# Kernel optimization log

Measured on AMD Instinct MI355X. Metric: run time of the kernel, lower is better.

The kernel has to match this reference:

```python
import jax, jax.numpy as jnp
import numpy as np

KH = KW = 3
STRIDE = 1
PAD = 1
DIL = 1
G = 4  # deformable groups


def setup_inputs() -> dict:
    key = jax.random.key(0)
    k1, k2, k3 = jax.random.split(key, 3)
    B, C, H, W = 8, 256, 64, 64
    K = KH * KW
    inp = jax.random.normal(k1, (B, C, H, W), dtype=jnp.float32)
    offset = jax.random.normal(k2, (B, 2 * G * K, H, W), dtype=jnp.float32)
    mask = jax.random.uniform(k3, (B, G * K, H, W), dtype=jnp.float32)
    return {"input": inp, "offset": offset, "mask": mask}


def _deform_sample(x, offset, mask):
    # x: [B,C,H,W]; offset: [B,2*G*K,Ho,Wo]; mask: [B,G*K,Ho,Wo]
    B, C, H, W = x.shape
    K = KH * KW
    Ho = (H + 2 * PAD - DIL * (KH - 1) - 1) // STRIDE + 1
    Wo = (W + 2 * PAD - DIL * (KW - 1) - 1) // STRIDE + 1
    Cg = C // G

    off = offset.reshape(B, G, K, 2, Ho, Wo)  # (dy, dx) per group/tap
    m = mask.reshape(B, G, K, Ho, Wo)

    # base sampling grid per kernel tap
    ky = (jnp.arange(KH) * DIL).repeat(KW)          # [K]
    kx = jnp.tile(jnp.arange(KW) * DIL, KH)          # [K]
    base_y = jnp.arange(Ho) * STRIDE - PAD           # [Ho]
    base_x = jnp.arange(Wo) * STRIDE - PAD           # [Wo]

    # sampling positions [B,G,K,Ho,Wo]
    py = base_y[None, None, None, :, None] + ky[None, None, :, None, None] + off[:, :, :, 0]
    px = base_x[None, None, None, None, :] + kx[None, None, :, None, None] + off[:, :, :, 1]

    y0 = jnp.floor(py).astype(jnp.int32)
    x0 = jnp.floor(px).astype(jnp.int32)
    ly = py - y0.astype(py.dtype)
    lx = px - x0.astype(px.dtype)

    xg = x.reshape(B, G, Cg, H * W)

    def gather(yy, xx, w):
        valid = (yy >= 0) & (yy < H) & (xx >= 0) & (xx < W)
        idx = jnp.clip(yy, 0, H - 1) * W + jnp.clip(xx, 0, W - 1)  # [B,G,K,Ho,Wo]
        g = jnp.take_along_axis(xg, idx.reshape(B, G, 1, -1), axis=3)
        g = g.reshape(B, G, Cg, K, Ho, Wo)
        return g * (w * valid.astype(w.dtype))[:, :, None]

    acc = gather(y0, x0, (1 - ly) * (1 - lx))
    acc = acc + gather(y0, x0 + 1, (1 - ly) * lx)
    acc = acc + gather(y0 + 1, x0, ly * (1 - lx))
    acc = acc + gather(y0 + 1, x0 + 1, ly * lx)

    # mask-weighted accumulation over kernel taps
    out = (acc * m[:, :, None]).sum(axis=3)  # [B,G,Cg,Ho,Wo]
    return out.reshape(B, C, Ho, Wo)


def reference(input, offset, mask):
    return _deform_sample(input, offset, mask)
```

## Files before the change

kernel.cpp:

```cpp
#include <hip/hip_runtime.h>
#include <hip/hip_fp16.h>

#define B_  8
#define C_  256
#define H_  64
#define W_  64
#define G_  4
#define CG_ 64
#define K_  9
#define HW_ (H_ * W_)

__global__ __launch_bounds__(256) void to_ghwc_f16(const float* __restrict__ in,
                                                   __half* __restrict__ out) {
  __shared__ unsigned int tile[32][65];
  const int b  = blockIdx.z;
  const int p0 = blockIdx.x * 64;
  const int g  = blockIdx.y;
  const int tid = threadIdx.x;
  const float* src = in + (size_t)b * C_ * HW_ + (size_t)g * CG_ * HW_;
  __half* dst = out + ((size_t)(b * G_ + g) * HW_) * CG_;

  const int px  = tid & 63;
  const int cp0 = tid >> 6;
#pragma unroll
  for (int i = 0; i < 8; ++i) {
    const int cp = cp0 + i * 4;
    const int c  = cp * 2;
    const float v0 = src[(size_t)c * HW_ + p0 + px];
    const float v1 = src[(size_t)(c + 1) * HW_ + p0 + px];
    const unsigned int lo = (unsigned int)__half_as_ushort(__float2half(v0));
    const unsigned int hi = (unsigned int)__half_as_ushort(__float2half(v1));
    tile[cp][px] = lo | (hi << 16);
  }
  __syncthreads();

  const int cpair = tid & 31;
  const int pr0   = tid >> 5;
#pragma unroll
  for (int i = 0; i < 8; ++i) {
    const int p = pr0 + i * 8;
    *(unsigned int*)(dst + (size_t)(p0 + p) * CG_ + 2 * cpair) = tile[cpair][p];
  }
}

union DeformSM {
  struct { int4 o[576]; float4 w[576]; } p;
  float ot[64][65];
};

__global__ __launch_bounds__(256) void deform_g16(const __half* __restrict__ x,
                                                  const float* __restrict__ off,
                                                  const float* __restrict__ msk,
                                                  float* __restrict__ out) {
  __shared__ DeformSM sm;

  const int ho  = blockIdx.x;
  const int b   = blockIdx.y >> 2;
  const int g   = blockIdx.y & 3;
  const int tid = threadIdx.x;

  for (int e = tid; e < 576; e += 256) {
    const int px = e & 63;
    const int k  = e >> 6;
    const int ky = k / 3, kx = k - ky * 3;
    const int och = (g * K_ + k) * 2;
    const size_t ob = ((size_t)(b * (2 * G_ * K_) + och) * HW_) + ho * W_ + px;
    const float dy = off[ob];
    const float dx = off[ob + HW_];
    const float m  = msk[((size_t)(b * (G_ * K_) + g * K_ + k) * HW_) + ho * W_ + px];

    const float py = (float)(ho - 1 + ky) + dy;
    const float pxx = (float)(px - 1 + kx) + dx;
    const float fy = floorf(py), fx = floorf(pxx);
    const int y0 = (int)fy, x0 = (int)fx;
    const int y1 = y0 + 1,  x1 = x0 + 1;
    const float ly = py - fy, lx = pxx - fx;

    const bool vy0 = ((unsigned)y0 < (unsigned)H_), vy1 = ((unsigned)y1 < (unsigned)H_);
    const bool vx0 = ((unsigned)x0 < (unsigned)W_), vx1 = ((unsigned)x1 < (unsigned)W_);
    const float wy0 = (1.f - ly) * m, wy1 = ly * m;

    float4 w;
    w.x = (vy0 && vx0) ? wy0 * (1.f - lx) : 0.f;
    w.y = (vy0 && vx1) ? wy0 * lx         : 0.f;
    w.z = (vy1 && vx0) ? wy1 * (1.f - lx) : 0.f;
    w.w = (vy1 && vx1) ? wy1 * lx         : 0.f;

    const int y0c = min(max(y0, 0), H_ - 1), y1c = min(max(y1, 0), H_ - 1);
    const int x0c = min(max(x0, 0), W_ - 1), x1c = min(max(x1, 0), W_ - 1);

    int4 o;
    o.x = (y0c * W_ + x0c) << 7;
    o.y = (y0c * W_ + x1c) << 7;
    o.z = (y1c * W_ + x0c) << 7;
    o.w = (y1c * W_ + x1c) << 7;
    sm.p.o[e] = o;
    sm.p.w[e] = w;
  }
  __syncthreads();

  const int ci = tid & 7;
  const int wi = tid >> 3;
  const char* xb = (const char*)x + (size_t)(b * G_ + g) * HW_ * CG_ * 2 + ci * 16;

  float a0[8] = {0.f, 0.f, 0.f, 0.f, 0.f, 0.f, 0.f, 0.f};
  float a1[8] = {0.f, 0.f, 0.f, 0.f, 0.f, 0.f, 0.f, 0.f};

#pragma unroll
  for (int k = 0; k < 9; ++k) {
    const int4   oA = sm.p.o[k * 64 + wi];
    const float4 wA = sm.p.w[k * 64 + wi];
    const int4   oB = sm.p.o[k * 64 + wi + 32];
    const float4 wB = sm.p.w[k * 64 + wi + 32];

    const float4 rA0 = *(const float4*)(xb + oA.x);
    const float4 rA1 = *(const float4*)(xb + oA.y);
    const float4 rA2 = *(const float4*)(xb + oA.z);
    const float4 rA3 = *(const float4*)(xb + oA.w);
    const float4 rB0 = *(const float4*)(xb + oB.x);
    const float4 rB1 = *(const float4*)(xb + oB.y);
    const float4 rB2 = *(const float4*)(xb + oB.z);
    const float4 rB3 = *(const float4*)(xb + oB.w);

    const __half* hA0 = (const __half*)&rA0;
    const __half* hA1 = (const __half*)&rA1;
    const __half* hA2 = (const __half*)&rA2;
    const __half* hA3 = (const __half*)&rA3;
    const __half* hB0 = (const __half*)&rB0;
    const __half* hB1 = (const __half*)&rB1;
    const __half* hB2 = (const __half*)&rB2;
    const __half* hB3 = (const __half*)&rB3;
#pragma unroll
    for (int j = 0; j < 8; ++j) {
      float s0 = a0[j];
      s0 = fmaf(wA.x, __half2float(hA0[j]), s0);
      s0 = fmaf(wA.y, __half2float(hA1[j]), s0);
      s0 = fmaf(wA.z, __half2float(hA2[j]), s0);
      s0 = fmaf(wA.w, __half2float(hA3[j]), s0);
      a0[j] = s0;
      float s1 = a1[j];
      s1 = fmaf(wB.x, __half2float(hB0[j]), s1);
      s1 = fmaf(wB.y, __half2float(hB1[j]), s1);
      s1 = fmaf(wB.z, __half2float(hB2[j]), s1);
      s1 = fmaf(wB.w, __half2float(hB3[j]), s1);
      a1[j] = s1;
    }
  }

  __syncthreads();
#pragma unroll
  for (int j = 0; j < 8; ++j) {
    sm.ot[ci * 8 + j][wi]      = a0[j];
    sm.ot[ci * 8 + j][wi + 32] = a1[j];
  }
  __syncthreads();

  float* ob = out + ((size_t)(b * C_ + g * CG_)) * HW_ + ho * W_;
  const int lane = tid & 63;
  const int r0   = tid >> 6;
#pragma unroll
  for (int q = 0; q < 16; ++q) {
    const int c = q * 4 + r0;
    ob[(size_t)c * HW_ + lane] = sm.ot[c][lane];
  }
}

__global__ __launch_bounds__(256) void deform_f32_nchw(const float* __restrict__ x,
                                                       const float* __restrict__ off,
                                                       const float* __restrict__ msk,
                                                       float* __restrict__ out) {
  __shared__ int4   s_o[144];
  __shared__ float4 s_w[144];
  const int woq = blockIdx.x;
  const int ho  = blockIdx.y;
  const int b   = blockIdx.z >> 2;
  const int g   = blockIdx.z & 3;
  const int tid = threadIdx.x;

  if (tid < 144) {
    const int wi = tid / 9, k = tid - wi * 9;
    const int wo = woq * 16 + wi;
    const int ky = k / 3, kx = k - ky * 3;
    const int och = (g * K_ + k) * 2;
    const size_t ob = ((size_t)(b * (2 * G_ * K_) + och) * H_ + ho) * W_ + wo;
    const float dy = off[ob];
    const float dx = off[ob + HW_];
    const float m  = msk[((size_t)(b * (G_ * K_) + g * K_ + k) * H_ + ho) * W_ + wo];
    const float py = (float)(ho - 1 + ky) + dy;
    const float px = (float)(wo - 1 + kx) + dx;
    const float fy = floorf(py), fx = floorf(px);
    const int y0 = (int)fy, x0 = (int)fx;
    const int y1 = y0 + 1,  x1 = x0 + 1;
    const float ly = py - fy, lx = px - fx;
    const bool vy0 = ((unsigned)y0 < (unsigned)H_), vy1 = ((unsigned)y1 < (unsigned)H_);
    const bool vx0 = ((unsigned)x0 < (unsigned)W_), vx1 = ((unsigned)x1 < (unsigned)W_);
    const float wy0 = (1.f - ly) * m, wy1 = ly * m;
    float4 w;
    w.x = (vy0 && vx0) ? wy0 * (1.f - lx) : 0.f;
    w.y = (vy0 && vx1) ? wy0 * lx         : 0.f;
    w.z = (vy1 && vx0) ? wy1 * (1.f - lx) : 0.f;
    w.w = (vy1 && vx1) ? wy1 * lx         : 0.f;
    const int y0c = min(max(y0, 0), H_ - 1), y1c = min(max(y1, 0), H_ - 1);
    const int x0c = min(max(x0, 0), W_ - 1), x1c = min(max(x1, 0), W_ - 1);
    s_o[tid] = make_int4(y0c * W_ + x0c, y0c * W_ + x1c, y1c * W_ + x0c, y1c * W_ + x1c);
    s_w[tid] = w;
  }
  __syncthreads();

  const int ci = tid & 15, wi = tid >> 4;
  const float* xb = x + (size_t)(b * C_ + g * CG_ + ci * 4) * HW_;
  float a0 = 0.f, a1 = 0.f, a2 = 0.f, a3 = 0.f;
#pragma unroll
  for (int k = 0; k < 9; ++k) {
    const int e = wi * 9 + k;
    const int4   o = s_o[e];
    const float4 w = s_w[e];
    a0 += w.x * xb[o.x] + w.y * xb[o.y] + w.z * xb[o.z] + w.w * xb[o.w];
    const float* x1p = xb + HW_;
    a1 += w.x * x1p[o.x] + w.y * x1p[o.y] + w.z * x1p[o.z] + w.w * x1p[o.w];
    const float* x2p = xb + 2 * HW_;
    a2 += w.x * x2p[o.x] + w.y * x2p[o.y] + w.z * x2p[o.z] + w.w * x2p[o.w];
    const float* x3p = xb + 3 * HW_;
    a3 += w.x * x3p[o.x] + w.y * x3p[o.y] + w.z * x3p[o.z] + w.w * x3p[o.w];
  }
  float* ob = out + ((size_t)(b * C_ + g * CG_ + ci * 4)) * HW_ + ho * W_ + woq * 16 + wi;
  ob[0] = a0; ob[HW_] = a1; ob[2 * HW_] = a2; ob[3 * HW_] = a3;
}

extern "C" void kernel_launch(void* const* d_in, const int* in_sizes, int n_in,
                              void* d_out, int out_size, void* d_ws, size_t ws_size,
                              hipStream_t stream) {
  const float* inp = (const float*)d_in[0];
  const float* off = (const float*)d_in[1];
  const float* msk = (const float*)d_in[2];
  float* out = (float*)d_out;

  const size_t need = (size_t)B_ * C_ * HW_ * sizeof(__half);
  if (ws_size >= need) {
    __half* xt = (__half*)d_ws;
    to_ghwc_f16<<<dim3(HW_ / 64, G_, B_), 256, 0, stream>>>(inp, xt);
    deform_g16<<<dim3(H_, B_ * G_), 256, 0, stream>>>(xt, off, msk, out);
  } else {
    deform_f32_nchw<<<dim3(4, H_, B_ * G_), 256, 0, stream>>>(inp, off, msk, out);
  }
}
```

Measured before the change: 45.93 us.

## Software-pipeline tap gathers, remap blocks across XCDs, and raise occupancy bound

The tap loop in the deform kernel now loads the next tap's offsets, weights and gathered fp16 rows before doing the current tap's FMAs, so gather latency overlaps with arithmetic. The grid becomes 1D and block ids are remapped so consecutive (b,g) rows land on the same XCD for L2 locality. Launch bounds now request 4 blocks per CU. Double-buffering the eight float4 gathers raises register pressure, and the occupancy hint may force spills.

```diff
diff --git a/kernel.cpp b/kernel.cpp
--- a/kernel.cpp
+++ b/kernel.cpp
@@ -48,15 +48,22 @@
   float ot[64][65];
 };
 
-__global__ __launch_bounds__(256) void deform_g16(const __half* __restrict__ x,
-                                                  const float* __restrict__ off,
-                                                  const float* __restrict__ msk,
-                                                  float* __restrict__ out) {
+__device__ __forceinline__ float4 ld16(const char* p, int off) {
+  return *(const float4*)(p + off);
+}
+
+__global__ __launch_bounds__(256, 4) void deform_g16(const __half* __restrict__ x,
+                                                     const float* __restrict__ off,
+                                                     const float* __restrict__ msk,
+                                                     float* __restrict__ out) {
   __shared__ DeformSM sm;
 
-  const int ho  = blockIdx.x;
-  const int b   = blockIdx.y >> 2;
-  const int g   = blockIdx.y & 3;
+  const int orig = blockIdx.x;
+  const int wgid = (orig & 7) * 256 + (orig >> 3);
+  const int ho = wgid & 63;
+  const int bg = wgid >> 6;
+  const int b  = bg >> 2;
+  const int g  = bg & 3;
   const int tid = threadIdx.x;
 
   for (int e = tid; e < 576; e += 256) {
@@ -69,7 +76,7 @@
     const float dx = off[ob + HW_];
     const float m  = msk[((size_t)(b * (G_ * K_) + g * K_ + k) * HW_) + ho * W_ + px];
 
-    const float py = (float)(ho - 1 + ky) + dy;
+    const float py  = (float)(ho - 1 + ky) + dy;
     const float pxx = (float)(px - 1 + kx) + dx;
     const float fy = floorf(py), fx = floorf(pxx);
     const int y0 = (int)fy, x0 = (int)fx;
@@ -106,21 +113,27 @@
   float a0[8] = {0.f, 0.f, 0.f, 0.f, 0.f, 0.f, 0.f, 0.f};
   float a1[8] = {0.f, 0.f, 0.f, 0.f, 0.f, 0.f, 0.f, 0.f};
 
+  float4 wA = sm.p.w[wi],      wB = sm.p.w[wi + 32];
+  int4   oA = sm.p.o[wi],      oB = sm.p.o[wi + 32];
+  float4 rA0 = ld16(xb, oA.x), rA1 = ld16(xb, oA.y);
+  float4 rA2 = ld16(xb, oA.z), rA3 = ld16(xb, oA.w);
+  float4 rB0 = ld16(xb, oB.x), rB1 = ld16(xb, oB.y);
+  float4 rB2 = ld16(xb, oB.z), rB3 = ld16(xb, oB.w);
+
 #pragma unroll
   for (int k = 0; k < 9; ++k) {
-    const int4   oA = sm.p.o[k * 64 + wi];
-    const float4 wA = sm.p.w[k * 64 + wi];
-    const int4   oB = sm.p.o[k * 64 + wi + 32];
-    const float4 wB = sm.p.w[k * 64 + wi + 32];
-
-    const float4 rA0 = *(const float4*)(xb + oA.x);
-    const float4 rA1 = *(const float4*)(xb + oA.y);
-    const float4 rA2 = *(const float4*)(xb + oA.z);
-    const float4 rA3 = *(const float4*)(xb + oA.w);
-    const float4 rB0 = *(const float4*)(xb + oB.x);
-    const float4 rB1 = *(const float4*)(xb + oB.y);
-    const float4 rB2 = *(const float4*)(xb + oB.z);
-    const float4 rB3 = *(const float4*)(xb + oB.w);
+    float4 nA0, nA1, nA2, nA3, nB0, nB1, nB2, nB3, nwA, nwB;
+    if (k < 8) {
+      const int e = (k + 1) * 64 + wi;
+      const int4 noA = sm.p.o[e];
+      const int4 noB = sm.p.o[e + 32];
+      nwA = sm.p.w[e];
+      nwB = sm.p.w[e + 32];
+      nA0 = ld16(xb, noA.x); nA1 = ld16(xb, noA.y);
+      nA2 = ld16(xb, noA.z); nA3 = ld16(xb, noA.w);
+      nB0 = ld16(xb, noB.x); nB1 = ld16(xb, noB.y);
+      nB2 = ld16(xb, noB.z); nB3 = ld16(xb, noB.w);
+    }
 
     const __half* hA0 = (const __half*)&rA0;
     const __half* hA1 = (const __half*)&rA1;
@@ -144,6 +157,12 @@
       s1 = fmaf(wB.z, __half2float(hB2[j]), s1);
       s1 = fmaf(wB.w, __half2float(hB3[j]), s1);
       a1[j] = s1;
+    }
+
+    if (k < 8) {
+      rA0 = nA0; rA1 = nA1; rA2 = nA2; rA3 = nA3;
+      rB0 = nB0; rB1 = nB1; rB2 = nB2; rB3 = nB3;
+      wA = nwA; wB = nwB;
     }
   }
 
@@ -239,7 +258,7 @@
   if (ws_size >= need) {
     __half* xt = (__half*)d_ws;
     to_ghwc_f16<<<dim3(HW_ / 64, G_, B_), 256, 0, stream>>>(inp, xt);
-    deform_g16<<<dim3(H_, B_ * G_), 256, 0, stream>>>(xt, off, msk, out);
+    deform_g16<<<dim3(H_ * B_ * G_), 256, 0, stream>>>(xt, off, msk, out);
   } else {
     deform_f32_nchw<<<dim3(4, H_, B_ * G_), 256, 0, stream>>>(inp, off, msk, out);
   }
```

After: 103.5 us. 125% more time.

## Remap deform blocks across XCDs for L2 locality and raise occupancy hint

Applied to the files above, without the earlier changes.

Flattens the deform kernel grid to 1D and swizzles the block index so that consecutive hardware-dispatched blocks, which round-robin over the 8 XCDs, map to contiguous (b,g,row) work on the same XCD. Neighbouring rows of the same image/group then share that XCD's L2 for the gathered fp16 input. It also adds a min-blocks-per-CU launch bound of 4 and restructures the gather address so the channel offset folds into the per-load offset. The added launch bound may constrain registers and cause spills.

```diff
diff --git a/kernel.cpp b/kernel.cpp
--- a/kernel.cpp
+++ b/kernel.cpp
@@ -48,15 +48,18 @@
   float ot[64][65];
 };
 
-__global__ __launch_bounds__(256) void deform_g16(const __half* __restrict__ x,
-                                                  const float* __restrict__ off,
-                                                  const float* __restrict__ msk,
-                                                  float* __restrict__ out) {
+__global__ __launch_bounds__(256, 4) void deform_g16(const __half* __restrict__ x,
+                                                     const float* __restrict__ off,
+                                                     const float* __restrict__ msk,
+                                                     float* __restrict__ out) {
   __shared__ DeformSM sm;
 
-  const int ho  = blockIdx.x;
-  const int b   = blockIdx.y >> 2;
-  const int g   = blockIdx.y & 3;
+  const int orig = blockIdx.x;
+  const int wgid = (orig & 7) * 256 + (orig >> 3);
+  const int ho = wgid & 63;
+  const int bg = wgid >> 6;
+  const int b  = bg >> 2;
+  const int g  = bg & 3;
   const int tid = threadIdx.x;
 
   for (int e = tid; e < 576; e += 256) {
@@ -69,7 +72,7 @@
     const float dx = off[ob + HW_];
     const float m  = msk[((size_t)(b * (G_ * K_) + g * K_ + k) * HW_) + ho * W_ + px];
 
-    const float py = (float)(ho - 1 + ky) + dy;
+    const float py  = (float)(ho - 1 + ky) + dy;
     const float pxx = (float)(px - 1 + kx) + dx;
     const float fy = floorf(py), fx = floorf(pxx);
     const int y0 = (int)fy, x0 = (int)fx;
@@ -99,9 +102,9 @@
   }
   __syncthreads();
 
-  const int ci = tid & 7;
-  const int wi = tid >> 3;
-  const char* xb = (const char*)x + (size_t)(b * G_ + g) * HW_ * CG_ * 2 + ci * 16;
+  const int ci16 = (tid & 7) * 16;
+  const int wi   = tid >> 3;
+  const char* base = (const char*)x + (size_t)(b * G_ + g) * (HW_ * CG_ * 2);
 
   float a0[8] = {0.f, 0.f, 0.f, 0.f, 0.f, 0.f, 0.f, 0.f};
   float a1[8] = {0.f, 0.f, 0.f, 0.f, 0.f, 0.f, 0.f, 0.f};
@@ -113,14 +116,14 @@
     const int4   oB = sm.p.o[k * 64 + wi + 32];
     const float4 wB = sm.p.w[k * 64 + wi + 32];
 
-    const float4 rA0 = *(const float4*)(xb + oA.x);
-    const float4 rA1 = *(const float4*)(xb + oA.y);
-    const float4 rA2 = *(const float4*)(xb + oA.z);
-    const float4 rA3 = *(const float4*)(xb + oA.w);
-    const float4 rB0 = *(const float4*)(xb + oB.x);
-    const float4 rB1 = *(const float4*)(xb + oB.y);
-    const float4 rB2 = *(const float4*)(xb + oB.z);
-    const float4 rB3 = *(const float4*)(xb + oB.w);
+    const float4 rA0 = *(const float4*)(base + (oA.x + ci16));
+    const float4 rA1 = *(const float4*)(base + (oA.y + ci16));
+    const float4 rA2 = *(const float4*)(base + (oA.z + ci16));
+    const float4 rA3 = *(const float4*)(base + (oA.w + ci16));
+    const float4 rB0 = *(const float4*)(base + (oB.x + ci16));
+    const float4 rB1 = *(const float4*)(base + (oB.y + ci16));
+    const float4 rB2 = *(const float4*)(base + (oB.z + ci16));
+    const float4 rB3 = *(const float4*)(base + (oB.w + ci16));
 
     const __half* hA0 = (const __half*)&rA0;
     const __half* hA1 = (const __half*)&rA1;
@@ -150,6 +153,7 @@
   __syncthreads();
 #pragma unroll
   for (int j = 0; j < 8; ++j) {
+    const int ci = tid & 7;
     sm.ot[ci * 8 + j][wi]      = a0[j];
     sm.ot[ci * 8 + j][wi + 32] = a1[j];
   }
@@ -239,7 +243,7 @@
   if (ws_size >= need) {
     __half* xt = (__half*)d_ws;
     to_ghwc_f16<<<dim3(HW_ / 64, G_, B_), 256, 0, stream>>>(inp, xt);
-    deform_g16<<<dim3(H_, B_ * G_), 256, 0, stream>>>(xt, off, msk, out);
+    deform_g16<<<dim3(H_ * B_ * G_), 256, 0, stream>>>(xt, off, msk, out);
   } else {
     deform_f32_nchw<<<dim3(4, H_, B_ * G_), 256, 0, stream>>>(inp, off, msk, out);
   }
```

Result: faster. 39.04 us (-15.0%).
